# Kernel optimization log

Hardware: AMD Instinct MI355X
Metric: run time of the kernel (lower is better)

Reference implementation:

```python
import jax, jax.numpy as jnp
import numpy as np

B, S, H, NH = 2, 2048, 1024, 16
DK = H // NH
EPS = 1e-12


def gelu(x):
    return x * jax.nn.sigmoid(1.702 * x)


def layer_norm(x, w, b):
    m = jnp.mean(x, axis=-1, keepdims=True)
    # torch.var default is unbiased (ddof=1)
    v = jnp.var(x, axis=-1, ddof=1, keepdims=True)
    return w * ((x - m) / jnp.sqrt(v + EPS)) + b


def setup_inputs() -> dict:
    key = jax.random.key(0)
    ks = jax.random.split(key, 20)
    sc = 1.0 / np.sqrt(H)
    d = {
        'batch_x': jax.random.normal(ks[0], (B, S, H), dtype=jnp.float32),
        'mask_x': jnp.ones((B, S), dtype=jnp.int32),
        'Wq': jax.random.normal(ks[1], (H, H), dtype=jnp.float32) * sc,
        'bq': jnp.zeros((H,), dtype=jnp.float32),
        'Wk': jax.random.normal(ks[2], (H, H), dtype=jnp.float32) * sc,
        'bk': jnp.zeros((H,), dtype=jnp.float32),
        'Wv': jax.random.normal(ks[3], (H, H), dtype=jnp.float32) * sc,
        'bv': jnp.zeros((H,), dtype=jnp.float32),
        'Wo': jax.random.normal(ks[4], (H, H), dtype=jnp.float32) * sc,
        'bo': jnp.zeros((H,), dtype=jnp.float32),
        'ln1_w': jax.random.normal(ks[5], (H,), dtype=jnp.float32),
        'ln1_b': jax.random.normal(ks[6], (H,), dtype=jnp.float32),
        'W1': jax.random.normal(ks[7], (H, H), dtype=jnp.float32) * sc,
        'b1': jnp.zeros((H,), dtype=jnp.float32),
        'W2': jax.random.normal(ks[8], (H, H), dtype=jnp.float32) * sc,
        'b2': jnp.zeros((H,), dtype=jnp.float32),
        'ln2_w': jax.random.normal(ks[9], (H,), dtype=jnp.float32),
        'ln2_b': jax.random.normal(ks[10], (H,), dtype=jnp.float32),
    }
    return d


def reference(batch_x, mask_x, Wq, bq, Wk, bk, Wv, bv, Wo, bo,
              ln1_w, ln1_b, W1, b1, W2, b2, ln2_w, ln2_b):
    bs, seq_len, hs = batch_x.shape
    # additive mask: padding AND causal (left2right -> lower-triangular)
    pad = mask_x[:, None, None, :].astype(jnp.int32)          # [B,1,1,S]
    causal = jnp.tril(jnp.ones((seq_len, seq_len), dtype=jnp.int32))[None, None]
    m = pad & causal                                          # [B,1,S,S]
    add_mask = ((1 - m) * -10000.0).astype(jnp.float32)

    # MHA
    Q = (batch_x @ Wq + bq).reshape(bs, seq_len, NH, DK)
    K = (batch_x @ Wk + bk).reshape(bs, seq_len, NH, DK)
    V = (batch_x @ Wv + bv).reshape(bs, seq_len, NH, DK)
    scores = jnp.einsum('bqhd,bkhd->bhqk', Q, K) / np.sqrt(DK) + add_mask
    proba = jax.nn.softmax(scores, axis=-1)
    attn = jnp.einsum('bhqk,bkhd->bqhd', proba, V).reshape(bs, seq_len, hs)
    attn = attn @ Wo + bo

    x = layer_norm(attn + batch_x, ln1_w, ln1_b)
    ff = gelu(x @ W1 + b1) @ W2 + b2
    return layer_norm(ff + x, ln2_w, ln2_b)
```

## Files before the change

kernel.cpp:

```cpp
#include <hip/hip_runtime.h>
#include <hip/hip_bf16.h>
#include <math.h>

#define BB    2
#define SEQ   2048
#define HID   1024
#define NHEAD 16
#define HDIM  64
#define ROWS  (BB*SEQ)

typedef __attribute__((ext_vector_type(8))) short bf16x8;
typedef __attribute__((ext_vector_type(4))) short bf16x4;
typedef __attribute__((ext_vector_type(4))) float f32x4;
typedef unsigned short ushort_t;

__device__ __forceinline__ unsigned short f2bf(float f) {
    unsigned int u = __float_as_uint(f);
    u += 0x7fffu + ((u >> 16) & 1u);
    return (unsigned short)(u >> 16);
}
__device__ __forceinline__ float bf2f(ushort_t u) {
    return __uint_as_float((unsigned int)u << 16);
}
__device__ __forceinline__ void gload16(const void* g, void* l) {
    __builtin_amdgcn_global_load_lds(
        (const __attribute__((address_space(1))) void*)g,
        (__attribute__((address_space(3))) void*)l, 16, 0, 0);
}

__global__ __launch_bounds__(256)
void cvt_bf16(const float* __restrict__ in, ushort_t* __restrict__ out)
{
    const int i = blockIdx.x * 256 + threadIdx.x;
    float4 v0 = ((const float4*)in)[2 * i];
    float4 v1 = ((const float4*)in)[2 * i + 1];
    bf16x8 o;
    o[0] = (short)f2bf(v0.x); o[1] = (short)f2bf(v0.y);
    o[2] = (short)f2bf(v0.z); o[3] = (short)f2bf(v0.w);
    o[4] = (short)f2bf(v1.x); o[5] = (short)f2bf(v1.y);
    o[6] = (short)f2bf(v1.z); o[7] = (short)f2bf(v1.w);
    ((bf16x8*)out)[i] = o;
}

__global__ __launch_bounds__(256)
void wtrans(const float* __restrict__ Wq, const float* __restrict__ Wk,
            const float* __restrict__ Wv, const float* __restrict__ Wo,
            const float* __restrict__ W1, const float* __restrict__ W2,
            ushort_t* __restrict__ Wt)
{
    __shared__ float t[64][65];
    const int z = blockIdx.z;
    const float* Win = z == 0 ? Wq : z == 1 ? Wk : z == 2 ? Wv
                     : z == 3 ? Wo : z == 4 ? W1 : W2;
    ushort_t* Wout = Wt + (size_t)z * (HID * HID);
    const int k0 = blockIdx.x * 64, n0 = blockIdx.y * 64;
    const int tid = threadIdx.x;
    const int r  = tid >> 2;
    const int cq = (tid & 3) * 16;

    #pragma unroll
    for (int c = 0; c < 16; c += 4) {
        float4 v = *(const float4*)&Win[(size_t)(k0 + r) * HID + n0 + cq + c];
        t[r][cq + c + 0] = v.x; t[r][cq + c + 1] = v.y;
        t[r][cq + c + 2] = v.z; t[r][cq + c + 3] = v.w;
    }
    __syncthreads();
    bf16x8 o0, o1;
    #pragma unroll
    for (int j = 0; j < 8; ++j) o0[j] = (short)f2bf(t[cq + j][r]);
    #pragma unroll
    for (int j = 0; j < 8; ++j) o1[j] = (short)f2bf(t[cq + 8 + j][r]);
    ushort_t* dst = Wout + (size_t)(n0 + r) * HID + k0 + cq;
    *(bf16x8*)&dst[0] = o0;
    *(bf16x8*)&dst[8] = o1;
}

__global__ __launch_bounds__(256)
void gemm_bf16(const ushort_t* __restrict__ A, const ushort_t* __restrict__ Bw,
               const float* __restrict__ b0, const float* __restrict__ b1,
               const float* __restrict__ b2,
               void* __restrict__ Y0, void* __restrict__ Y1, void* __restrict__ Y2,
               int mode)
{
    __shared__ __align__(16) ushort_t As_s[128 * 64];
    __shared__ __align__(16) ushort_t Bs_s[128 * 64];

    const int tid  = threadIdx.x;
    const int lane = tid & 63;
    const int w    = tid >> 6;
    const int lr   = lane & 15;
    const int lg   = lane >> 4;
    const int wrow = (w >> 1) * 64;
    const int wcol = (w & 1) * 64;
    const int m0   = blockIdx.y * 128;
    const int n0g  = blockIdx.x * 128;
    const int sel  = n0g >> 10;
    const int n0   = n0g & 1023;

    const int srow = lane >> 3;
    size_t aoff[4], boff[4];
    int lofs[4];
    #pragma unroll
    for (int i = 0; i < 4; ++i) {
        const int rl = w * 32 + i * 8 + srow;
        const int gc = (lane & 7) ^ (rl & 7);
        aoff[i] = (size_t)(m0  + rl) * HID + (gc << 3);
        boff[i] = (size_t)(n0g + rl) * HID + (gc << 3);
        lofs[i] = (w * 32 + i * 8) * 64;
    }

    f32x4 acc[4][4];
    #pragma unroll
    for (int i = 0; i < 4; ++i)
        #pragma unroll
        for (int j = 0; j < 4; ++j) acc[i][j] = (f32x4){0.f, 0.f, 0.f, 0.f};

    for (int k0 = 0; k0 < HID; k0 += 64) {
        #pragma unroll
        for (int i = 0; i < 4; ++i) gload16(A  + aoff[i] + k0, &As_s[lofs[i]]);
        #pragma unroll
        for (int i = 0; i < 4; ++i) gload16(Bw + boff[i] + k0, &Bs_s[lofs[i]]);
        __syncthreads();

        #pragma unroll
        for (int kf = 0; kf < 2; ++kf) {
            const int c = kf * 4 + lg;
            bf16x8 a[4], b[4];
            #pragma unroll
            for (int i = 0; i < 4; ++i) {
                const int row = wrow + i * 16 + lr;
                a[i] = *(const bf16x8*)&As_s[row * 64 + ((c ^ (row & 7)) << 3)];
            }
            #pragma unroll
            for (int j = 0; j < 4; ++j) {
                const int col = wcol + j * 16 + lr;
                b[j] = *(const bf16x8*)&Bs_s[col * 64 + ((c ^ (col & 7)) << 3)];
            }
            #pragma unroll
            for (int i = 0; i < 4; ++i)
                #pragma unroll
                for (int j = 0; j < 4; ++j)
                    acc[i][j] = __builtin_amdgcn_mfma_f32_16x16x32_bf16(a[i], b[j], acc[i][j], 0, 0, 0);
        }
        __syncthreads();
    }

    if (mode == 2) {
        if (sel < 2) {
            ushort_t* Yb = (ushort_t*)(sel == 0 ? Y0 : Y1);
            const float* bp = sel == 0 ? b0 : b1;
            #pragma unroll
            for (int i = 0; i < 4; ++i)
                #pragma unroll
                for (int j = 0; j < 4; ++j) {
                    const int col = n0 + wcol + j * 16 + lr;
                    const float bb = bp[col];
                    #pragma unroll
                    for (int r = 0; r < 4; ++r) {
                        const int row = m0 + wrow + i * 16 + lg * 4 + r;
                        Yb[(size_t)row * HID + col] = f2bf(acc[i][j][r] + bb);
                    }
                }
        } else {
            ushort_t* Yt = (ushort_t*)Y2;
            const int bq = m0 >> 11;
            #pragma unroll
            for (int i = 0; i < 4; ++i)
                #pragma unroll
                for (int j = 0; j < 4; ++j) {
                    const int col = n0 + wcol + j * 16 + lr;
                    const float bb = b2[col];
                    bf16x4 pk;
                    #pragma unroll
                    for (int r = 0; r < 4; ++r) pk[r] = (short)f2bf(acc[i][j][r] + bb);
                    size_t idx = (size_t)bq * (NHEAD * HDIM * SEQ)
                               + (size_t)col * SEQ + (m0 & 2047) + wrow + i * 16 + lg * 4;
                    *(bf16x4*)&Yt[idx] = pk;
                }
        }
    } else if (mode == 1) {
        ushort_t* Yb = (ushort_t*)Y0;
        #pragma unroll
        for (int i = 0; i < 4; ++i)
            #pragma unroll
            for (int j = 0; j < 4; ++j) {
                const int col = n0 + wcol + j * 16 + lr;
                const float bb = b0[col];
                #pragma unroll
                for (int r = 0; r < 4; ++r) {
                    const int row = m0 + wrow + i * 16 + lg * 4 + r;
                    float v = acc[i][j][r] + bb;
                    v = v / (1.f + __expf(-1.702f * v));
                    Yb[(size_t)row * HID + col] = f2bf(v);
                }
            }
    } else {
        float* Yf = (float*)Y0;
        #pragma unroll
        for (int i = 0; i < 4; ++i)
            #pragma unroll
            for (int j = 0; j < 4; ++j) {
                const int col = n0 + wcol + j * 16 + lr;
                const float bb = b0[col];
                #pragma unroll
                for (int r = 0; r < 4; ++r) {
                    const int row = m0 + wrow + i * 16 + lg * 4 + r;
                    Yf[(size_t)row * HID + col] = acc[i][j][r] + bb;
                }
            }
    }
}

__global__ __launch_bounds__(256)
void attn_mfma(const ushort_t* __restrict__ Qb, const ushort_t* __restrict__ Kb,
               const ushort_t* __restrict__ Vt, ushort_t* __restrict__ O)
{
    __shared__ __align__(16) ushort_t Q_lds[64 * 64];
    __shared__ __align__(16) ushort_t K_lds[64 * 64];
    __shared__ __align__(16) ushort_t V_lds[64 * 64];
    __shared__ __align__(16) ushort_t P_lds[4][16 * 64];

    const int tid  = threadIdx.x;
    const int lane = tid & 63;
    const int w    = tid >> 6;
    const int lr   = lane & 15;
    const int lg   = lane >> 4;

    const int qt = gridDim.x - 1 - blockIdx.x;
    const int h  = blockIdx.y;
    const int b  = blockIdx.z;

    const ushort_t* Qg = Qb + ((size_t)(b * SEQ + qt * 64)) * HID + h * HDIM;
    #pragma unroll
    for (int u = 0; u < 2; ++u) {
        int unit = u * 256 + tid;
        int row  = unit >> 3;
        int c8   = (unit & 7) << 3;
        bf16x8 v = *(const bf16x8*)(Qg + (size_t)row * HID + c8);
        *(bf16x8*)&Q_lds[row * 64 + (c8 ^ ((row & 7) << 3))] = v;
    }
    __syncthreads();

    bf16x8 qf[2];
    {
        const int row = w * 16 + lr;
        qf[0] = *(const bf16x8*)&Q_lds[row * 64 + ((lg * 8) ^ ((row & 7) << 3))];
        qf[1] = *(const bf16x8*)&Q_lds[row * 64 + ((32 + lg * 8) ^ ((row & 7) << 3))];
    }

    f32x4 oacc[4];
    #pragma unroll
    for (int d = 0; d < 4; ++d) oacc[d] = (f32x4){0.f, 0.f, 0.f, 0.f};
    float mrow[4] = {-1e30f, -1e30f, -1e30f, -1e30f};
    float lrow[4] = {0.f, 0.f, 0.f, 0.f};

    const int qloc = w * 16 + lg * 4;
    const ushort_t* Kg0 = Kb + ((size_t)(b * SEQ)) * HID + h * HDIM;
    const ushort_t* Vg0 = Vt + ((size_t)(b * NHEAD + h) * HDIM) * SEQ;

    for (int kt = 0; kt <= qt; ++kt) {
        __syncthreads();
        const ushort_t* Kg = Kg0 + (size_t)(kt * 64) * HID;
        const ushort_t* Vg = Vg0 + kt * 64;
        #pragma unroll
        for (int u = 0; u < 2; ++u) {
            int unit = u * 256 + tid;
            int row  = unit >> 3;
            int c8   = (unit & 7) << 3;
            int swz  = c8 ^ ((row & 7) << 3);
            bf16x8 kv = *(const bf16x8*)(Kg + (size_t)row * HID + c8);
            *(bf16x8*)&K_lds[row * 64 + swz] = kv;
            bf16x8 vv = *(const bf16x8*)(Vg + (size_t)row * SEQ + c8);
            *(bf16x8*)&V_lds[row * 64 + swz] = vv;
        }
        __syncthreads();

        f32x4 sacc[4];
        #pragma unroll
        for (int s = 0; s < 4; ++s) {
            const int col = s * 16 + lr;
            bf16x8 k0 = *(const bf16x8*)&K_lds[col * 64 + ((lg * 8) ^ ((col & 7) << 3))];
            bf16x8 k1 = *(const bf16x8*)&K_lds[col * 64 + ((32 + lg * 8) ^ ((col & 7) << 3))];
            f32x4 z = (f32x4){0.f, 0.f, 0.f, 0.f};
            z = __builtin_amdgcn_mfma_f32_16x16x32_bf16(qf[0], k0, z, 0, 0, 0);
            z = __builtin_amdgcn_mfma_f32_16x16x32_bf16(qf[1], k1, z, 0, 0, 0);
            sacc[s] = z;
        }

        const bool diag = (kt == qt);
        #pragma unroll
        for (int s = 0; s < 4; ++s) {
            const int key = s * 16 + lr;
            #pragma unroll
            for (int r = 0; r < 4; ++r) {
                float v = sacc[s][r] * 0.125f;
                if (diag && key > qloc + r) v = -1e30f;
                sacc[s][r] = v;
            }
        }

        float corr[4];
        #pragma unroll
        for (int r = 0; r < 4; ++r) {
            float mt = fmaxf(fmaxf(sacc[0][r], sacc[1][r]), fmaxf(sacc[2][r], sacc[3][r]));
            mt = fmaxf(mt, __shfl_xor(mt, 1));
            mt = fmaxf(mt, __shfl_xor(mt, 2));
            mt = fmaxf(mt, __shfl_xor(mt, 4));
            mt = fmaxf(mt, __shfl_xor(mt, 8));
            const float mnew = fmaxf(mrow[r], mt);
            const float c = __expf(mrow[r] - mnew);
            float p0 = __expf(sacc[0][r] - mnew);
            float p1 = __expf(sacc[1][r] - mnew);
            float p2 = __expf(sacc[2][r] - mnew);
            float p3 = __expf(sacc[3][r] - mnew);
            sacc[0][r] = p0; sacc[1][r] = p1; sacc[2][r] = p2; sacc[3][r] = p3;
            float ps = (p0 + p1) + (p2 + p3);
            ps += __shfl_xor(ps, 1);
            ps += __shfl_xor(ps, 2);
            ps += __shfl_xor(ps, 4);
            ps += __shfl_xor(ps, 8);
            lrow[r] = fmaf(lrow[r], c, ps);
            mrow[r] = mnew;
            corr[r] = c;
        }
        #pragma unroll
        for (int d = 0; d < 4; ++d)
            #pragma unroll
            for (int r = 0; r < 4; ++r) oacc[d][r] *= corr[r];

        #pragma unroll
        for (int s = 0; s < 4; ++s) {
            unsigned int pk0, pk1;
            asm("v_cvt_pk_bf16_f32 %0, %1, %2" : "=v"(pk0) : "v"(sacc[s][0]), "v"(sacc[s][1]));
            asm("v_cvt_pk_bf16_f32 %0, %1, %2" : "=v"(pk1) : "v"(sacc[s][2]), "v"(sacc[s][3]));
            const int key = s * 16 + lr;
            const int r0 = lg * 4;
            P_lds[w][(r0 + 0) * 64 + (key ^ (((r0 + 0) & 7) << 3))] = (ushort_t)(pk0 & 0xffff);
            P_lds[w][(r0 + 1) * 64 + (key ^ (((r0 + 1) & 7) << 3))] = (ushort_t)(pk0 >> 16);
            P_lds[w][(r0 + 2) * 64 + (key ^ (((r0 + 2) & 7) << 3))] = (ushort_t)(pk1 & 0xffff);
            P_lds[w][(r0 + 3) * 64 + (key ^ (((r0 + 3) & 7) << 3))] = (ushort_t)(pk1 >> 16);
        }

        bf16x8 pa0 = *(const bf16x8*)&P_lds[w][lr * 64 + ((lg * 8) ^ ((lr & 7) << 3))];
        bf16x8 pa1 = *(const bf16x8*)&P_lds[w][lr * 64 + ((32 + lg * 8) ^ ((lr & 7) << 3))];
        #pragma unroll
        for (int d = 0; d < 4; ++d) {
            const int col = d * 16 + lr;
            bf16x8 v0 = *(const bf16x8*)&V_lds[col * 64 + ((lg * 8) ^ ((col & 7) << 3))];
            bf16x8 v1 = *(const bf16x8*)&V_lds[col * 64 + ((32 + lg * 8) ^ ((col & 7) << 3))];
            oacc[d] = __builtin_amdgcn_mfma_f32_16x16x32_bf16(pa0, v0, oacc[d], 0, 0, 0);
            oacc[d] = __builtin_amdgcn_mfma_f32_16x16x32_bf16(pa1, v1, oacc[d], 0, 0, 0);
        }
    }

    float inv[4];
    #pragma unroll
    for (int r = 0; r < 4; ++r) inv[r] = 1.f / lrow[r];
    ushort_t* Og = O + ((size_t)(b * SEQ + qt * 64 + w * 16)) * HID + h * HDIM;
    #pragma unroll
    for (int d = 0; d < 4; ++d)
        #pragma unroll
        for (int r = 0; r < 4; ++r)
            Og[(size_t)(lg * 4 + r) * HID + d * 16 + lr] = f2bf(oacc[d][r] * inv[r]);
}

__global__ __launch_bounds__(256)
void ln_res_bf16(const float* __restrict__ Xa, const float* __restrict__ Xb,
                 const float* __restrict__ w, const float* __restrict__ bia,
                 ushort_t* __restrict__ Y)
{
    const int row = blockIdx.x;
    const int t   = threadIdx.x;
    const size_t off = (size_t)row * HID + (t << 2);

    float4 xa = *(const float4*)&Xa[off];
    float4 xb = *(const float4*)&Xb[off];
    float x0 = xa.x + xb.x, x1 = xa.y + xb.y, x2 = xa.z + xb.z, x3 = xa.w + xb.w;

    float sum = x0 + x1 + x2 + x3;
    float ss  = x0 * x0 + x1 * x1 + x2 * x2 + x3 * x3;
    #pragma unroll
    for (int o = 32; o > 0; o >>= 1) {
        sum += __shfl_down(sum, o);
        ss  += __shfl_down(ss, o);
    }
    __shared__ float s1[4], s2[4];
    __shared__ float mean_s, rstd_s;
    if ((t & 63) == 0) { s1[t >> 6] = sum; s2[t >> 6] = ss; }
    __syncthreads();
    if (t == 0) {
        float S1 = s1[0] + s1[1] + s1[2] + s1[3];
        float S2 = s2[0] + s2[1] + s2[2] + s2[3];
        float m  = S1 / (float)HID;
        float var = (S2 - (float)HID * m * m) / (float)(HID - 1);
        mean_s = m;
        rstd_s = rsqrtf(var + 1e-12f);
    }
    __syncthreads();
    const float m = mean_s, rs = rstd_s;

    float4 wv = *(const float4*)&w[t << 2];
    float4 bv = *(const float4*)&bia[t << 2];
    bf16x4 o;
    o[0] = (short)f2bf(wv.x * ((x0 - m) * rs) + bv.x);
    o[1] = (short)f2bf(wv.y * ((x1 - m) * rs) + bv.y);
    o[2] = (short)f2bf(wv.z * ((x2 - m) * rs) + bv.z);
    o[3] = (short)f2bf(wv.w * ((x3 - m) * rs) + bv.w);
    *(bf16x4*)&Y[off] = o;
}

__global__ __launch_bounds__(256)
void ln_res_out(const float* __restrict__ Xa, const ushort_t* __restrict__ Xr,
                const float* __restrict__ w, const float* __restrict__ bia,
                float* __restrict__ Y)
{
    const int row = blockIdx.x;
    const int t   = threadIdx.x;
    const size_t off = (size_t)row * HID + (t << 2);

    float4 xa = *(const float4*)&Xa[off];
    bf16x4 rb = *(const bf16x4*)&Xr[off];
    float x0 = xa.x + bf2f((ushort_t)rb[0]);
    float x1 = xa.y + bf2f((ushort_t)rb[1]);
    float x2 = xa.z + bf2f((ushort_t)rb[2]);
    float x3 = xa.w + bf2f((ushort_t)rb[3]);

    float sum = x0 + x1 + x2 + x3;
    float ss  = x0 * x0 + x1 * x1 + x2 * x2 + x3 * x3;
    #pragma unroll
    for (int o = 32; o > 0; o >>= 1) {
        sum += __shfl_down(sum, o);
        ss  += __shfl_down(ss, o);
    }
    __shared__ float s1[4], s2[4];
    __shared__ float mean_s, rstd_s;
    if ((t & 63) == 0) { s1[t >> 6] = sum; s2[t >> 6] = ss; }
    __syncthreads();
    if (t == 0) {
        float S1 = s1[0] + s1[1] + s1[2] + s1[3];
        float S2 = s2[0] + s2[1] + s2[2] + s2[3];
        float m  = S1 / (float)HID;
        float var = (S2 - (float)HID * m * m) / (float)(HID - 1);
        mean_s = m;
        rstd_s = rsqrtf(var + 1e-12f);
    }
    __syncthreads();
    const float m = mean_s, rs = rstd_s;

    float4 wv = *(const float4*)&w[t << 2];
    float4 bv = *(const float4*)&bia[t << 2];
    float4 y;
    y.x = wv.x * ((x0 - m) * rs) + bv.x;
    y.y = wv.y * ((x1 - m) * rs) + bv.y;
    y.z = wv.z * ((x2 - m) * rs) + bv.z;
    y.w = wv.w * ((x3 - m) * rs) + bv.w;
    *(float4*)&Y[off] = y;
}

extern "C" void kernel_launch(void* const* d_in, const int* in_sizes, int n_in,
                              void* d_out, int out_size, void* d_ws, size_t ws_size,
                              hipStream_t stream)
{
    const float* X    = (const float*)d_in[0];
    const float* Wq   = (const float*)d_in[2];
    const float* bq   = (const float*)d_in[3];
    const float* Wk   = (const float*)d_in[4];
    const float* bk   = (const float*)d_in[5];
    const float* Wv   = (const float*)d_in[6];
    const float* bv   = (const float*)d_in[7];
    const float* Wo   = (const float*)d_in[8];
    const float* bo   = (const float*)d_in[9];
    const float* ln1w = (const float*)d_in[10];
    const float* ln1b = (const float*)d_in[11];
    const float* W1   = (const float*)d_in[12];
    const float* b1   = (const float*)d_in[13];
    const float* W2   = (const float*)d_in[14];
    const float* b2   = (const float*)d_in[15];
    const float* ln2w = (const float*)d_in[16];
    const float* ln2b = (const float*)d_in[17];
    float* out = (float*)d_out;

    const size_t EL = (size_t)ROWS * HID;
    const size_t WEL = (size_t)HID * HID;
    ushort_t* wsu = (ushort_t*)d_ws;
    ushort_t* Xb  = wsu;
    ushort_t* Wt  = Xb + EL;
    ushort_t* Qb  = Wt + 6 * WEL;
    ushort_t* Kb  = Qb + EL;
    ushort_t* Vtb = Kb + EL;
    ushort_t* Ob  = Xb;
    float*    P   = (float*)Qb;
    ushort_t* x1b = Vtb;
    ushort_t* g   = Xb;
    float*    ff2 = P;

    dim3 gb(256);

    cvt_bf16<<<dim3(EL / (256 * 8)), gb, 0, stream>>>(X, Xb);
    wtrans<<<dim3(16, 16, 6), gb, 0, stream>>>(Wq, Wk, Wv, Wo, W1, W2, Wt);

    gemm_bf16<<<dim3(24, ROWS / 128), gb, 0, stream>>>(
        Xb, Wt, bq, bk, bv, Qb, Kb, Vtb, 2);
    attn_mfma<<<dim3(SEQ / 64, NHEAD, BB), gb, 0, stream>>>(Qb, Kb, Vtb, Ob);
    gemm_bf16<<<dim3(8, ROWS / 128), gb, 0, stream>>>(
        Ob, Wt + 3 * WEL, bo, bo, bo, P, P, P, 0);
    ln_res_bf16<<<dim3(ROWS), gb, 0, stream>>>(P, X, ln1w, ln1b, x1b);
    gemm_bf16<<<dim3(8, ROWS / 128), gb, 0, stream>>>(
        x1b, Wt + 4 * WEL, b1, b1, b1, g, g, g, 1);
    gemm_bf16<<<dim3(8, ROWS / 128), gb, 0, stream>>>(
        g, Wt + 5 * WEL, b2, b2, b2, ff2, ff2, ff2, 0);
    ln_res_out<<<dim3(ROWS), gb, 0, stream>>>(ff2, x1b, ln2w, ln2b, out);
}
```

Before: 372.8 us.

## Pair causal query tiles per block and double-buffer K/V with async LDS loads

The attention kernel now launches 16 blocks per head instead of 32. Each block handles two query tiles, qt = 31-i and qt = i, so every block does the same amount of causal work. K and V tiles are double-buffered in LDS and loaded with gload16 (global-to-LDS), so the next tile is prefetched while the current one is computed on. This removes one barrier per iteration and aims to hide load latency and causal load imbalance. In exchange, LDS use rises and grid parallelism halves (512 blocks), which may lower occupancy or CU coverage.

```diff
diff --git a/kernel.cpp b/kernel.cpp
--- a/kernel.cpp
+++ b/kernel.cpp
@@ -216,8 +216,8 @@
                const ushort_t* __restrict__ Vt, ushort_t* __restrict__ O)
 {
     __shared__ __align__(16) ushort_t Q_lds[64 * 64];
-    __shared__ __align__(16) ushort_t K_lds[64 * 64];
-    __shared__ __align__(16) ushort_t V_lds[64 * 64];
+    __shared__ __align__(16) ushort_t K_lds[2][64 * 64];
+    __shared__ __align__(16) ushort_t V_lds[2][64 * 64];
     __shared__ __align__(16) ushort_t P_lds[4][16 * 64];
 
     const int tid  = threadIdx.x;
@@ -226,142 +226,164 @@
     const int lr   = lane & 15;
     const int lg   = lane >> 4;
 
-    const int qt = gridDim.x - 1 - blockIdx.x;
-    const int h  = blockIdx.y;
-    const int b  = blockIdx.z;
-
-    const ushort_t* Qg = Qb + ((size_t)(b * SEQ + qt * 64)) * HID + h * HDIM;
-    #pragma unroll
-    for (int u = 0; u < 2; ++u) {
-        int unit = u * 256 + tid;
-        int row  = unit >> 3;
-        int c8   = (unit & 7) << 3;
-        bf16x8 v = *(const bf16x8*)(Qg + (size_t)row * HID + c8);
-        *(bf16x8*)&Q_lds[row * 64 + (c8 ^ ((row & 7) << 3))] = v;
-    }
-    __syncthreads();
-
-    bf16x8 qf[2];
-    {
-        const int row = w * 16 + lr;
-        qf[0] = *(const bf16x8*)&Q_lds[row * 64 + ((lg * 8) ^ ((row & 7) << 3))];
-        qf[1] = *(const bf16x8*)&Q_lds[row * 64 + ((32 + lg * 8) ^ ((row & 7) << 3))];
-    }
-
-    f32x4 oacc[4];
-    #pragma unroll
-    for (int d = 0; d < 4; ++d) oacc[d] = (f32x4){0.f, 0.f, 0.f, 0.f};
-    float mrow[4] = {-1e30f, -1e30f, -1e30f, -1e30f};
-    float lrow[4] = {0.f, 0.f, 0.f, 0.f};
-
-    const int qloc = w * 16 + lg * 4;
+    const int h = blockIdx.y;
+    const int b = blockIdx.z;
+
     const ushort_t* Kg0 = Kb + ((size_t)(b * SEQ)) * HID + h * HDIM;
     const ushort_t* Vg0 = Vt + ((size_t)(b * NHEAD + h) * HDIM) * SEQ;
 
-    for (int kt = 0; kt <= qt; ++kt) {
+    const int srow = lane >> 3;
+    const int schk = lane & 7;
+    size_t koff[2], voff[2];
+    int lofs[2];
+    #pragma unroll
+    for (int u = 0; u < 2; ++u) {
+        const int row = w * 16 + u * 8 + srow;
+        const int gc  = schk ^ (row & 7);
+        koff[u] = (size_t)row * HID + (gc << 3);
+        voff[u] = (size_t)row * SEQ + (gc << 3);
+        lofs[u] = (w * 16 + u * 8) * 64;
+    }
+
+    const int qloc = w * 16 + lg * 4;
+
+    for (int half = 0; half < 2; ++half) {
+        const int qt = half ? blockIdx.x : 31 - blockIdx.x;
+
         __syncthreads();
-        const ushort_t* Kg = Kg0 + (size_t)(kt * 64) * HID;
-        const ushort_t* Vg = Vg0 + kt * 64;
+
+        #pragma unroll
+        for (int u = 0; u < 2; ++u) {
+            gload16(Kg0 + koff[u], &K_lds[0][lofs[u]]);
+            gload16(Vg0 + voff[u], &V_lds[0][lofs[u]]);
+        }
+        const ushort_t* Qg = Qb + ((size_t)(b * SEQ + qt * 64)) * HID + h * HDIM;
         #pragma unroll
         for (int u = 0; u < 2; ++u) {
             int unit = u * 256 + tid;
             int row  = unit >> 3;
             int c8   = (unit & 7) << 3;
-            int swz  = c8 ^ ((row & 7) << 3);
-            bf16x8 kv = *(const bf16x8*)(Kg + (size_t)row * HID + c8);
-            *(bf16x8*)&K_lds[row * 64 + swz] = kv;
-            bf16x8 vv = *(const bf16x8*)(Vg + (size_t)row * SEQ + c8);
-            *(bf16x8*)&V_lds[row * 64 + swz] = vv;
+            bf16x8 v = *(const bf16x8*)(Qg + (size_t)row * HID + c8);
+            *(bf16x8*)&Q_lds[row * 64 + (c8 ^ ((row & 7) << 3))] = v;
         }
         __syncthreads();
 
-        f32x4 sacc[4];
-        #pragma unroll
-        for (int s = 0; s < 4; ++s) {
-            const int col = s * 16 + lr;
-            bf16x8 k0 = *(const bf16x8*)&K_lds[col * 64 + ((lg * 8) ^ ((col & 7) << 3))];
-            bf16x8 k1 = *(const bf16x8*)&K_lds[col * 64 + ((32 + lg * 8) ^ ((col & 7) << 3))];
-            f32x4 z = (f32x4){0.f, 0.f, 0.f, 0.f};
-            z = __builtin_amdgcn_mfma_f32_16x16x32_bf16(qf[0], k0, z, 0, 0, 0);
-            z = __builtin_amdgcn_mfma_f32_16x16x32_bf16(qf[1], k1, z, 0, 0, 0);
-            sacc[s] = z;
+        bf16x8 qf[2];
+        {
+            const int row = w * 16 + lr;
+            qf[0] = *(const bf16x8*)&Q_lds[row * 64 + ((lg * 8) ^ ((row & 7) << 3))];
+            qf[1] = *(const bf16x8*)&Q_lds[row * 64 + ((32 + lg * 8) ^ ((row & 7) << 3))];
         }
 
-        const bool diag = (kt == qt);
-        #pragma unroll
-        for (int s = 0; s < 4; ++s) {
-            const int key = s * 16 + lr;
+        f32x4 oacc[4];
+        #pragma unroll
+        for (int d = 0; d < 4; ++d) oacc[d] = (f32x4){0.f, 0.f, 0.f, 0.f};
+        float mrow[4] = {-1e30f, -1e30f, -1e30f, -1e30f};
+        float lrow[4] = {0.f, 0.f, 0.f, 0.f};
+
+        int cur = 0;
+        for (int kt = 0; kt <= qt; ++kt) {
+            if (kt > 0) __syncthreads();
+            if (kt < qt) {
+                const ushort_t* Kg = Kg0 + (size_t)((kt + 1) * 64) * HID;
+                const ushort_t* Vg = Vg0 + (kt + 1) * 64;
+                const int nb = cur ^ 1;
+                #pragma unroll
+                for (int u = 0; u < 2; ++u) {
+                    gload16(Kg + koff[u], &K_lds[nb][lofs[u]]);
+                    gload16(Vg + voff[u], &V_lds[nb][lofs[u]]);
+                }
+            }
+
+            f32x4 sacc[4];
+            #pragma unroll
+            for (int s = 0; s < 4; ++s) {
+                const int col = s * 16 + lr;
+                bf16x8 k0 = *(const bf16x8*)&K_lds[cur][col * 64 + ((lg * 8) ^ ((col & 7) << 3))];
+                bf16x8 k1 = *(const bf16x8*)&K_lds[cur][col * 64 + ((32 + lg * 8) ^ ((col & 7) << 3))];
+                f32x4 z = (f32x4){0.f, 0.f, 0.f, 0.f};
+                z = __builtin_amdgcn_mfma_f32_16x16x32_bf16(qf[0], k0, z, 0, 0, 0);
+                z = __builtin_amdgcn_mfma_f32_16x16x32_bf16(qf[1], k1, z, 0, 0, 0);
+                sacc[s] = z;
+            }
+
+            const bool diag = (kt == qt);
+            #pragma unroll
+            for (int s = 0; s < 4; ++s) {
+                const int key = s * 16 + lr;
+                #pragma unroll
+                for (int r = 0; r < 4; ++r) {
+                    float v = sacc[s][r] * 0.125f;
+                    if (diag && key > qloc + r) v = -1e30f;
+                    sacc[s][r] = v;
+                }
+            }
+
+            float corr[4];
             #pragma unroll
             for (int r = 0; r < 4; ++r) {
-                float v = sacc[s][r] * 0.125f;
-                if (diag && key > qloc + r) v = -1e30f;
-                sacc[s][r] = v;
-            }
+                float mt = fmaxf(fmaxf(sacc[0][r], sacc[1][r]), fmaxf(sacc[2][r], sacc[3][r]));
+                mt = fmaxf(mt, __shfl_xor(mt, 1));
+                mt = fmaxf(mt, __shfl_xor(mt, 2));
+                mt = fmaxf(mt, __shfl_xor(mt, 4));
+                mt = fmaxf(mt, __shfl_xor(mt, 8));
+                const float mnew = fmaxf(mrow[r], mt);
+                const float c = __expf(mrow[r] - mnew);
+                float p0 = __expf(sacc[0][r] - mnew);
+                float p1 = __expf(sacc[1][r] - mnew);
+                float p2 = __expf(sacc[2][r] - mnew);
+                float p3 = __expf(sacc[3][r] - mnew);
+                sacc[0][r] = p0; sacc[1][r] = p1; sacc[2][r] = p2; sacc[3][r] = p3;
+                float ps = (p0 + p1) + (p2 + p3);
+                ps += __shfl_xor(ps, 1);
+                ps += __shfl_xor(ps, 2);
+                ps += __shfl_xor(ps, 4);
+                ps += __shfl_xor(ps, 8);
+                lrow[r] = fmaf(lrow[r], c, ps);
+                mrow[r] = mnew;
+                corr[r] = c;
+            }
+            #pragma unroll
+            for (int d = 0; d < 4; ++d)
+                #pragma unroll
+                for (int r = 0; r < 4; ++r) oacc[d][r] *= corr[r];
+
+            #pragma unroll
+            for (int s = 0; s < 4; ++s) {
+                unsigned int pk0, pk1;
+                asm("v_cvt_pk_bf16_f32 %0, %1, %2" : "=v"(pk0) : "v"(sacc[s][0]), "v"(sacc[s][1]));
+                asm("v_cvt_pk_bf16_f32 %0, %1, %2" : "=v"(pk1) : "v"(sacc[s][2]), "v"(sacc[s][3]));
+                const int key = s * 16 + lr;
+                const int r0 = lg * 4;
+                P_lds[w][(r0 + 0) * 64 + (key ^ (((r0 + 0) & 7) << 3))] = (ushort_t)(pk0 & 0xffff);
+                P_lds[w][(r0 + 1) * 64 + (key ^ (((r0 + 1) & 7) << 3))] = (ushort_t)(pk0 >> 16);
+                P_lds[w][(r0 + 2) * 64 + (key ^ (((r0 + 2) & 7) << 3))] = (ushort_t)(pk1 & 0xffff);
+                P_lds[w][(r0 + 3) * 64 + (key ^ (((r0 + 3) & 7) << 3))] = (ushort_t)(pk1 >> 16);
+            }
+
+            bf16x8 pa0 = *(const bf16x8*)&P_lds[w][lr * 64 + ((lg * 8) ^ ((lr & 7) << 3))];
+            bf16x8 pa1 = *(const bf16x8*)&P_lds[w][lr * 64 + ((32 + lg * 8) ^ ((lr & 7) << 3))];
+            #pragma unroll
+            for (int d = 0; d < 4; ++d) {
+                const int col = d * 16 + lr;
+                bf16x8 v0 = *(const bf16x8*)&V_lds[cur][col * 64 + ((lg * 8) ^ ((col & 7) << 3))];
+                bf16x8 v1 = *(const bf16x8*)&V_lds[cur][col * 64 + ((32 + lg * 8) ^ ((col & 7) << 3))];
+                oacc[d] = __builtin_amdgcn_mfma_f32_16x16x32_bf16(pa0, v0, oacc[d], 0, 0, 0);
+                oacc[d] = __builtin_amdgcn_mfma_f32_16x16x32_bf16(pa1, v1, oacc[d], 0, 0, 0);
+            }
+            cur ^= 1;
         }
 
-        float corr[4];
-        #pragma unroll
-        for (int r = 0; r < 4; ++r) {
-            float mt = fmaxf(fmaxf(sacc[0][r], sacc[1][r]), fmaxf(sacc[2][r], sacc[3][r]));
-            mt = fmaxf(mt, __shfl_xor(mt, 1));
-            mt = fmaxf(mt, __shfl_xor(mt, 2));
-            mt = fmaxf(mt, __shfl_xor(mt, 4));
-            mt = fmaxf(mt, __shfl_xor(mt, 8));
-            const float mnew = fmaxf(mrow[r], mt);
-            const float c = __expf(mrow[r] - mnew);
-            float p0 = __expf(sacc[0][r] - mnew);
-            float p1 = __expf(sacc[1][r] - mnew);
-            float p2 = __expf(sacc[2][r] - mnew);
-            float p3 = __expf(sacc[3][r] - mnew);
-            sacc[0][r] = p0; sacc[1][r] = p1; sacc[2][r] = p2; sacc[3][r] = p3;
-            float ps = (p0 + p1) + (p2 + p3);
-            ps += __shfl_xor(ps, 1);
-            ps += __shfl_xor(ps, 2);
-            ps += __shfl_xor(ps, 4);
-            ps += __shfl_xor(ps, 8);
-            lrow[r] = fmaf(lrow[r], c, ps);
-            mrow[r] = mnew;
-            corr[r] = c;
-        }
+        float inv[4];
+        #pragma unroll
+        for (int r = 0; r < 4; ++r) inv[r] = 1.f / lrow[r];
+        ushort_t* Og = O + ((size_t)(b * SEQ + qt * 64 + w * 16)) * HID + h * HDIM;
         #pragma unroll
         for (int d = 0; d < 4; ++d)
             #pragma unroll
-            for (int r = 0; r < 4; ++r) oacc[d][r] *= corr[r];
-
-        #pragma unroll
-        for (int s = 0; s < 4; ++s) {
-            unsigned int pk0, pk1;
-            asm("v_cvt_pk_bf16_f32 %0, %1, %2" : "=v"(pk0) : "v"(sacc[s][0]), "v"(sacc[s][1]));
-            asm("v_cvt_pk_bf16_f32 %0, %1, %2" : "=v"(pk1) : "v"(sacc[s][2]), "v"(sacc[s][3]));
-            const int key = s * 16 + lr;
-            const int r0 = lg * 4;
-            P_lds[w][(r0 + 0) * 64 + (key ^ (((r0 + 0) & 7) << 3))] = (ushort_t)(pk0 & 0xffff);
-            P_lds[w][(r0 + 1) * 64 + (key ^ (((r0 + 1) & 7) << 3))] = (ushort_t)(pk0 >> 16);
-            P_lds[w][(r0 + 2) * 64 + (key ^ (((r0 + 2) & 7) << 3))] = (ushort_t)(pk1 & 0xffff);
-            P_lds[w][(r0 + 3) * 64 + (key ^ (((r0 + 3) & 7) << 3))] = (ushort_t)(pk1 >> 16);
-        }
-
-        bf16x8 pa0 = *(const bf16x8*)&P_lds[w][lr * 64 + ((lg * 8) ^ ((lr & 7) << 3))];
-        bf16x8 pa1 = *(const bf16x8*)&P_lds[w][lr * 64 + ((32 + lg * 8) ^ ((lr & 7) << 3))];
-        #pragma unroll
-        for (int d = 0; d < 4; ++d) {
-            const int col = d * 16 + lr;
-            bf16x8 v0 = *(const bf16x8*)&V_lds[col * 64 + ((lg * 8) ^ ((col & 7) << 3))];
-            bf16x8 v1 = *(const bf16x8*)&V_lds[col * 64 + ((32 + lg * 8) ^ ((col & 7) << 3))];
-            oacc[d] = __builtin_amdgcn_mfma_f32_16x16x32_bf16(pa0, v0, oacc[d], 0, 0, 0);
-            oacc[d] = __builtin_amdgcn_mfma_f32_16x16x32_bf16(pa1, v1, oacc[d], 0, 0, 0);
-        }
-    }
-
-    float inv[4];
-    #pragma unroll
-    for (int r = 0; r < 4; ++r) inv[r] = 1.f / lrow[r];
-    ushort_t* Og = O + ((size_t)(b * SEQ + qt * 64 + w * 16)) * HID + h * HDIM;
-    #pragma unroll
-    for (int d = 0; d < 4; ++d)
-        #pragma unroll
-        for (int r = 0; r < 4; ++r)
-            Og[(size_t)(lg * 4 + r) * HID + d * 16 + lr] = f2bf(oacc[d][r] * inv[r]);
+            for (int r = 0; r < 4; ++r)
+                Og[(size_t)(lg * 4 + r) * HID + d * 16 + lr] = f2bf(oacc[d][r] * inv[r]);
+    }
 }
 
 __global__ __launch_bounds__(256)
@@ -501,7 +523,7 @@
 
     gemm_bf16<<<dim3(24, ROWS / 128), gb, 0, stream>>>(
         Xb, Wt, bq, bk, bv, Qb, Kb, Vtb, 2);
-    attn_mfma<<<dim3(SEQ / 64, NHEAD, BB), gb, 0, stream>>>(Qb, Kb, Vtb, Ob);
+    attn_mfma<<<dim3(16, NHEAD, BB), gb, 0, stream>>>(Qb, Kb, Vtb, Ob);
     gemm_bf16<<<dim3(8, ROWS / 128), gb, 0, stream>>>(
         Ob, Wt + 3 * WEL, bo, bo, bo, P, P, P, 0);
     ln_res_bf16<<<dim3(ROWS), gb, 0, stream>>>(P, X, ln1w, ln1b, x1b);
```

After: 320.7 us. 14.0% less time.
